# Performance work log

Measured on AMD Instinct MI355X. Metric: run time of the kernel, lower is better.

Reference implementation:

```python
import jax, jax.numpy as jnp
import numpy as np

N = 200000   # number of nodes / adj columns
F = 256      # input_features
L0 = 256     # layers[0]
L1 = 128     # layers[1]


def setup_inputs() -> dict:
    key = jax.random.key(0)
    k_adj, k_feat, k0, kb0, k1, kb1, ks = jax.random.split(key, 7)
    adj = jax.random.randint(k_adj, (1, N), 0, 2, dtype=jnp.int32)
    feature = jax.random.normal(k_feat, (N, F), dtype=jnp.float32)
    # MLP params: Linear(2F, L0) -> relu -> Linear(L0, L1) -> relu; score Linear(L1, 1, bias=False)
    W0 = jax.random.normal(k0, (2 * F, L0), dtype=jnp.float32) * 0.02
    b0 = jax.random.normal(kb0, (L0,), dtype=jnp.float32) * 0.02
    W1 = jax.random.normal(k1, (L0, L1), dtype=jnp.float32) * 0.02
    b1 = jax.random.normal(kb1, (L1,), dtype=jnp.float32) * 0.02
    w_score = jax.random.normal(ks, (L1, 1), dtype=jnp.float32) * 0.02
    return {"adj": adj, "feature": feature, "W0": W0, "b0": b0,
            "W1": W1, "b1": b1, "w_score": w_score}


def reference(adj, feature, W0, b0, W1, b1, w_score):
    # Original forward only processes row i=0 of adj (loop breaks immediately).
    # idx = nonzero columns of adj[0], plus sentinel -233 at the end.
    # Neighbor feature is feature[v] if v > 0 else zeros (so column 0 and the
    # sentinel both get a zero vector). Softmax is over the neighbor set (dim 0);
    # we realize this as a masked softmax over all N columns + 1 sentinel slot.
    n, f = feature.shape
    row = adj[0]
    mask = jnp.concatenate([row != 0, jnp.ones((1,), dtype=bool)])  # [n+1]
    # neighbor features: feature[v] for v=0..n-1 (v=0 -> zeros), plus zero sentinel row
    neigh = jnp.concatenate([feature.at[0].set(0.0),
                             jnp.zeros((1, f), feature.dtype)], axis=0)  # [n+1, f]
    self_feat = jnp.broadcast_to(feature[0], (n + 1, f))                 # [n+1, f]
    s = jnp.concatenate([self_feat, neigh], axis=1)                      # [n+1, 2f]
    h = jax.nn.relu(s @ W0 + b0)                                         # [n+1, L0]
    h = jax.nn.relu(h @ W1 + b1)                                         # [n+1, L1]
    scores = h @ w_score                                                 # [n+1, 1]
    scores = jnp.where(mask[:, None], scores, jnp.float32(-1e30))
    lk = jax.nn.softmax(scores, axis=0)
    return jnp.where(mask[:, None], lk, 0.0)
```

## Files before the change

### kernel.cpp

```cpp
#include <hip/hip_runtime.h>
#include <stdint.h>

#define NN   200000
#define NTOT 200001

typedef short bf16x8 __attribute__((ext_vector_type(8)));
typedef float f32x16 __attribute__((ext_vector_type(16)));

union FragU { bf16x8 v; unsigned q[4]; };

__device__ __forceinline__ unsigned bfrne(float x) {
  unsigned u = __float_as_uint(x);
  return (u + 0x7fffu + ((u >> 16) & 1u)) >> 16;
}
__device__ __forceinline__ unsigned pk2(float a, float b) {
  return bfrne(a) | (bfrne(b) << 16);
}
__device__ __forceinline__ unsigned shx32(unsigned x) {
  return (unsigned)__shfl_xor((int)x, 32, 64);
}

__global__ void gnn_prep(const float* __restrict__ feat, const float* __restrict__ W0,
                         const float* __restrict__ b0, const float* __restrict__ W1,
                         const float* __restrict__ b1, const float* __restrict__ wsc,
                         float* __restrict__ c0g, char* __restrict__ w0t,
                         char* __restrict__ w1t, float* __restrict__ scores,
                         float* __restrict__ S, int* __restrict__ cnt)
{
  const int tid = threadIdx.x;
  if (blockIdx.x == 0) {
    __shared__ float h0z[256];
    __shared__ float h1z[128];
    float a = b0[tid];
    for (int f = 0; f < 256; ++f) a = fmaf(feat[f], W0[f * 256 + tid], a);
    c0g[tid] = a;
    h0z[tid] = fmaxf(a, 0.f);
    __syncthreads();
    if (tid < 128) {
      float t = b1[tid];
      for (int k = 0; k < 256; ++k) t = fmaf(h0z[k], W1[k * 128 + tid], t);
      h1z[tid] = fmaxf(t, 0.f) * wsc[tid];
    }
    __syncthreads();
    if (tid == 0) {
      float sz = 0.f;
      for (int p = 0; p < 128; ++p) sz += h1z[p];
      scores[0]  = sz;
      scores[NN] = sz;
      *S = 0.f;
      *cnt = 0;
    }
  } else {
    int gid = (blockIdx.x - 1) * 256 + tid;
    if (gid < 8192) {
      int m = gid >> 5, a = gid & 31, k0 = a * 8;
      unsigned q0 = pk2(W0[(256 + k0 + 0) * 256 + m], W0[(256 + k0 + 1) * 256 + m]);
      unsigned q1 = pk2(W0[(256 + k0 + 2) * 256 + m], W0[(256 + k0 + 3) * 256 + m]);
      unsigned q2 = pk2(W0[(256 + k0 + 4) * 256 + m], W0[(256 + k0 + 5) * 256 + m]);
      unsigned q3 = pk2(W0[(256 + k0 + 6) * 256 + m], W0[(256 + k0 + 7) * 256 + m]);
      *(uint4*)(w0t + m * 512 + ((a ^ (m & 7)) << 4)) = make_uint4(q0, q1, q2, q3);
    } else if (gid < 12288) {
      int g2 = gid - 8192;
      int p = g2 >> 5, a = g2 & 31, k0 = a * 8;
      unsigned q0 = pk2(W1[(k0 + 0) * 128 + p], W1[(k0 + 1) * 128 + p]);
      unsigned q1 = pk2(W1[(k0 + 2) * 128 + p], W1[(k0 + 3) * 128 + p]);
      unsigned q2 = pk2(W1[(k0 + 4) * 128 + p], W1[(k0 + 5) * 128 + p]);
      unsigned q3 = pk2(W1[(k0 + 6) * 128 + p], W1[(k0 + 7) * 128 + p]);
      *(uint4*)(w1t + p * 512 + ((a ^ (p & 7)) << 4)) = make_uint4(q0, q1, q2, q3);
    }
  }
}

__global__ void gnn_compact(const int* __restrict__ adj, int* __restrict__ idx,
                            int* __restrict__ cnt)
{
  int i = blockIdx.x * blockDim.x + threadIdx.x;
  bool f = (i > 0) && (i < NN) && (adj[i] != 0);
  unsigned long long m = __ballot(f);
  int lane = threadIdx.x & 63;
  int tot = __popcll(m);
  int base = 0;
  if (lane == 0 && tot) base = atomicAdd(cnt, tot);
  base = __shfl(base, 0, 64);
  if (f) idx[base + __popcll(m & ((1ull << lane) - 1ull))] = i;
}

__global__ __launch_bounds__(256, 2) void
gnn_main(const float* __restrict__ feat, const char* __restrict__ w0t,
         const char* __restrict__ w1t, const float* __restrict__ c0g,
         const float* __restrict__ b1, const float* __restrict__ wsc,
         const int* __restrict__ idx, const int* __restrict__ cnt,
         float* __restrict__ scores)
{
  __shared__ __align__(16) char sW[2][32768];
  __shared__ float c0s[256];
  __shared__ float b1s[128];
  __shared__ float wss[128];

  const int M = *cnt;
  if ((int)blockIdx.x * 128 >= M) return;

  const int tid  = threadIdx.x;
  const int wave = tid >> 6, lane = tid & 63;
  const int h = lane >> 5, nl = lane & 31;

  const int slot = blockIdx.x * 128 + wave * 32 + nl;
  const int node = idx[min(slot, M - 1)];

  auto stage = [&](int buf, const char* gsrc) {
    const char* gp = gsrc + (wave << 13) + (lane << 4);
    char* lp = &sW[buf][wave << 13];
#pragma unroll
    for (int i = 0; i < 8; ++i)
      __builtin_amdgcn_global_load_lds(
          (const __attribute__((address_space(1))) unsigned*)(gp + (i << 10)),
          (__attribute__((address_space(3))) unsigned*)(lp + (i << 10)),
          16, 0, 0);
  };

  stage(0, w0t);

  FragU fB[16];
  const float4* frow = (const float4*)(feat + (size_t)node * 256);
#pragma unroll
  for (int kk = 0; kk < 16; ++kk) {
    float4 x = frow[4 * kk + 2 * h];
    float4 y = frow[4 * kk + 2 * h + 1];
    fB[kk].q[0] = pk2(x.x, x.y);
    fB[kk].q[1] = pk2(x.z, x.w);
    fB[kk].q[2] = pk2(y.x, y.y);
    fB[kk].q[3] = pk2(y.z, y.w);
  }

  c0s[tid] = c0g[tid];
  if (tid < 128) { b1s[tid] = b1[tid]; wss[tid] = wsc[tid]; }
  __syncthreads();

  unsigned h0p[8][8];
#pragma unroll
  for (int c = 0; c < 4; ++c) {
    stage((c + 1) & 1, (c < 3) ? (w0t + (c + 1) * 32768) : w1t);
    const char* Bp = sW[c & 1];
    f32x16 acc0, acc1;
#pragma unroll
    for (int i = 0; i < 16; ++i) { acc0[i] = 0.f; acc1[i] = 0.f; }
#pragma unroll
    for (int kk = 0; kk < 16; ++kk) {
      bf16x8 a0 = *(const bf16x8*)(Bp + nl * 512        + (((2 * kk + h) ^ (nl & 7)) << 4));
      bf16x8 a1 = *(const bf16x8*)(Bp + (32 + nl) * 512 + (((2 * kk + h) ^ (nl & 7)) << 4));
      acc0 = __builtin_amdgcn_mfma_f32_32x32x16_bf16(a0, fB[kk].v, acc0, 0, 0, 0);
      acc1 = __builtin_amdgcn_mfma_f32_32x32x16_bf16(a1, fB[kk].v, acc1, 0, 0, 0);
    }
#pragma unroll
    for (int t = 0; t < 2; ++t) {
      const f32x16& ac = t ? acc1 : acc0;
      const int tile = c * 2 + t, nb = tile * 32;
#pragma unroll
      for (int g = 0; g < 4; ++g) {
        float4 cv = *(const float4*)&c0s[nb + 8 * g + 4 * h];
        float v0 = fmaxf(ac[4 * g + 0] + cv.x, 0.f);
        float v1 = fmaxf(ac[4 * g + 1] + cv.y, 0.f);
        float v2 = fmaxf(ac[4 * g + 2] + cv.z, 0.f);
        float v3 = fmaxf(ac[4 * g + 3] + cv.w, 0.f);
        h0p[tile][2 * g + 0] = pk2(v0, v1);
        h0p[tile][2 * g + 1] = pk2(v2, v3);
      }
    }
    __syncthreads();
  }

  const bool hh = (h != 0);
#pragma unroll
  for (int tt = 0; tt < 8; ++tt) {
    unsigned o[8], s[8];
#pragma unroll
    for (int r = 0; r < 8; ++r) { o[r] = h0p[tt][r]; s[r] = shx32(o[r]); }
    h0p[tt][0] = hh ? s[2] : o[0];
    h0p[tt][1] = hh ? s[3] : o[1];
    h0p[tt][2] = hh ? o[2] : s[0];
    h0p[tt][3] = hh ? o[3] : s[1];
    h0p[tt][4] = hh ? s[6] : o[4];
    h0p[tt][5] = hh ? s[7] : o[5];
    h0p[tt][6] = hh ? o[6] : s[4];
    h0p[tt][7] = hh ? o[7] : s[5];
  }

  f32x16 acc2[4];
#pragma unroll
  for (int t = 0; t < 4; ++t)
#pragma unroll
    for (int i = 0; i < 16; ++i) acc2[t][i] = 0.f;

#pragma unroll
  for (int c2 = 0; c2 < 2; ++c2) {
    if (c2 == 0) stage(1, w1t + 32768);
    const char* Bp = sW[c2];
#pragma unroll
    for (int kk = 0; kk < 16; ++kk) {
      bf16x8 a0 = *(const bf16x8*)(Bp + nl * 512        + (((2 * kk + h) ^ (nl & 7)) << 4));
      bf16x8 a1 = *(const bf16x8*)(Bp + (32 + nl) * 512 + (((2 * kk + h) ^ (nl & 7)) << 4));
      FragU bb;
      const int tt = kk >> 1, p = kk & 1;
      bb.q[0] = h0p[tt][4 * p + 0];
      bb.q[1] = h0p[tt][4 * p + 1];
      bb.q[2] = h0p[tt][4 * p + 2];
      bb.q[3] = h0p[tt][4 * p + 3];
      acc2[c2 * 2 + 0] = __builtin_amdgcn_mfma_f32_32x32x16_bf16(a0, bb.v, acc2[c2 * 2 + 0], 0, 0, 0);
      acc2[c2 * 2 + 1] = __builtin_amdgcn_mfma_f32_32x32x16_bf16(a1, bb.v, acc2[c2 * 2 + 1], 0, 0, 0);
    }
    if (c2 == 0) __syncthreads();
  }

  float sc = 0.f;
#pragma unroll
  for (int pt = 0; pt < 4; ++pt) {
#pragma unroll
    for (int g = 0; g < 4; ++g) {
      float4 bv = *(const float4*)&b1s[pt * 32 + 8 * g + 4 * h];
      float4 wv = *(const float4*)&wss[pt * 32 + 8 * g + 4 * h];
      sc += fmaxf(acc2[pt][4 * g + 0] + bv.x, 0.f) * wv.x;
      sc += fmaxf(acc2[pt][4 * g + 1] + bv.y, 0.f) * wv.y;
      sc += fmaxf(acc2[pt][4 * g + 2] + bv.z, 0.f) * wv.z;
      sc += fmaxf(acc2[pt][4 * g + 3] + bv.w, 0.f) * wv.w;
    }
  }
  sc += __shfl_xor(sc, 32, 64);
  if (h == 0 && slot < M) scores[node] = sc;
}

__global__ void gnn_reduce(const int* __restrict__ adj, const float* __restrict__ scores,
                           float* __restrict__ S)
{
  float loc = 0.f;
  for (int i = blockIdx.x * blockDim.x + threadIdx.x; i <= NN;
       i += gridDim.x * blockDim.x) {
    bool m = (i == NN) || (adj[i] != 0);
    if (m) loc += expf(scores[i]);
  }
#pragma unroll
  for (int off = 32; off; off >>= 1) loc += __shfl_xor(loc, off, 64);
  __shared__ float part[4];
  if ((threadIdx.x & 63) == 0) part[threadIdx.x >> 6] = loc;
  __syncthreads();
  if (threadIdx.x == 0) atomicAdd(S, part[0] + part[1] + part[2] + part[3]);
}

__global__ void gnn_final(const int* __restrict__ adj, const float* __restrict__ scores,
                          const float* __restrict__ S, float* __restrict__ out)
{
  int i = blockIdx.x * blockDim.x + threadIdx.x;
  if (i > NN) return;
  bool m = (i == NN) || (adj[i] != 0);
  float Sv = *S;
  out[i] = m ? expf(scores[i]) / Sv : 0.f;
}

extern "C" void kernel_launch(void* const* d_in, const int* in_sizes, int n_in,
                              void* d_out, int out_size, void* d_ws, size_t ws_size,
                              hipStream_t stream)
{
  (void)in_sizes; (void)n_in; (void)out_size; (void)ws_size;
  const int*   adj  = (const int*)d_in[0];
  const float* feat = (const float*)d_in[1];
  const float* W0   = (const float*)d_in[2];
  const float* b0   = (const float*)d_in[3];
  const float* W1   = (const float*)d_in[4];
  const float* b1   = (const float*)d_in[5];
  const float* wsc  = (const float*)d_in[6];
  float* out = (float*)d_out;

  char* ws = (char*)d_ws;
  float* scores = (float*)ws;
  char*  w0t    = ws + 800256;
  char*  w1t    = ws + 931328;
  float* c0g    = (float*)(ws + 996864);
  float* S      = (float*)(ws + 997888);
  int*   cnt    = (int*)(ws + 997904);
  int*   idxb   = (int*)(ws + 997952);

  gnn_prep   <<<49,   256, 0, stream>>>(feat, W0, b0, W1, b1, wsc, c0g, w0t, w1t, scores, S, cnt);
  gnn_compact<<<782,  256, 0, stream>>>(adj, idxb, cnt);
  gnn_main   <<<1563, 256, 0, stream>>>(feat, w0t, w1t, c0g, b1, wsc, idxb, cnt, scores);
  gnn_reduce <<<512,  256, 0, stream>>>(adj, scores, S);
  gnn_final  <<<782,  256, 0, stream>>>(adj, scores, S, out);
}
```

Measured before the change: 365.3 us.

## Fuse softmax denominator into main kernel, permute W1 layout, batch compaction

```diff
diff --git a/kernel.cpp b/kernel.cpp
--- a/kernel.cpp
+++ b/kernel.cpp
@@ -16,16 +16,14 @@
 __device__ __forceinline__ unsigned pk2(float a, float b) {
   return bfrne(a) | (bfrne(b) << 16);
 }
-__device__ __forceinline__ unsigned shx32(unsigned x) {
-  return (unsigned)__shfl_xor((int)x, 32, 64);
-}
-
-__global__ void gnn_prep(const float* __restrict__ feat, const float* __restrict__ W0,
-                         const float* __restrict__ b0, const float* __restrict__ W1,
-                         const float* __restrict__ b1, const float* __restrict__ wsc,
-                         float* __restrict__ c0g, char* __restrict__ w0t,
-                         char* __restrict__ w1t, float* __restrict__ scores,
-                         float* __restrict__ S, int* __restrict__ cnt)
+
+__global__ void gnn_prep(const int* __restrict__ adj, const float* __restrict__ feat,
+                         const float* __restrict__ W0, const float* __restrict__ b0,
+                         const float* __restrict__ W1, const float* __restrict__ b1,
+                         const float* __restrict__ wsc, float* __restrict__ c0g,
+                         char* __restrict__ w0t, char* __restrict__ w1t,
+                         float* __restrict__ scores, float* __restrict__ S,
+                         int* __restrict__ cnt)
 {
   const int tid = threadIdx.x;
   if (blockIdx.x == 0) {
@@ -47,7 +45,7 @@
       for (int p = 0; p < 128; ++p) sz += h1z[p];
       scores[0]  = sz;
       scores[NN] = sz;
-      *S = 0.f;
+      *S = expf(sz) * (adj[0] != 0 ? 2.f : 1.f);
       *cnt = 0;
     }
   } else {
@@ -61,28 +59,52 @@
       *(uint4*)(w0t + m * 512 + ((a ^ (m & 7)) << 4)) = make_uint4(q0, q1, q2, q3);
     } else if (gid < 12288) {
       int g2 = gid - 8192;
-      int p = g2 >> 5, a = g2 & 31, k0 = a * 8;
-      unsigned q0 = pk2(W1[(k0 + 0) * 128 + p], W1[(k0 + 1) * 128 + p]);
-      unsigned q1 = pk2(W1[(k0 + 2) * 128 + p], W1[(k0 + 3) * 128 + p]);
-      unsigned q2 = pk2(W1[(k0 + 4) * 128 + p], W1[(k0 + 5) * 128 + p]);
-      unsigned q3 = pk2(W1[(k0 + 6) * 128 + p], W1[(k0 + 7) * 128 + p]);
+      int p = g2 >> 5, a = g2 & 31;
+      int base = 32 * (a >> 2) + 16 * ((a >> 1) & 1) + 4 * (a & 1);
+      unsigned q0 = pk2(W1[(base + 0)  * 128 + p], W1[(base + 1)  * 128 + p]);
+      unsigned q1 = pk2(W1[(base + 2)  * 128 + p], W1[(base + 3)  * 128 + p]);
+      unsigned q2 = pk2(W1[(base + 8)  * 128 + p], W1[(base + 9)  * 128 + p]);
+      unsigned q3 = pk2(W1[(base + 10) * 128 + p], W1[(base + 11) * 128 + p]);
       *(uint4*)(w1t + p * 512 + ((a ^ (p & 7)) << 4)) = make_uint4(q0, q1, q2, q3);
     }
   }
 }
 
-__global__ void gnn_compact(const int* __restrict__ adj, int* __restrict__ idx,
-                            int* __restrict__ cnt)
-{
-  int i = blockIdx.x * blockDim.x + threadIdx.x;
-  bool f = (i > 0) && (i < NN) && (adj[i] != 0);
-  unsigned long long m = __ballot(f);
-  int lane = threadIdx.x & 63;
-  int tot = __popcll(m);
-  int base = 0;
-  if (lane == 0 && tot) base = atomicAdd(cnt, tot);
-  base = __shfl(base, 0, 64);
-  if (f) idx[base + __popcll(m & ((1ull << lane) - 1ull))] = i;
+__global__ __launch_bounds__(1024) void
+gnn_compact(const int* __restrict__ adj, int* __restrict__ idx, int* __restrict__ cnt)
+{
+  __shared__ int wc[64];
+  __shared__ int bbase;
+  const int tid  = threadIdx.x;
+  const int wave = tid >> 6, lane = tid & 63;
+  const int R = blockIdx.x * 4096;
+
+  unsigned long long mk[4];
+#pragma unroll
+  for (int p = 0; p < 4; ++p) {
+    int i = R + p * 1024 + tid;
+    bool f = (i > 0) && (i < NN) && (adj[i] != 0);
+    mk[p] = __ballot(f);
+  }
+  if (lane == 0) {
+#pragma unroll
+    for (int p = 0; p < 4; ++p) wc[p * 16 + wave] = __popcll(mk[p]);
+  }
+  __syncthreads();
+  if (tid == 0) {
+    int run = 0;
+    for (int e = 0; e < 64; ++e) { int v = wc[e]; wc[e] = run; run += v; }
+    bbase = atomicAdd(cnt, run);
+  }
+  __syncthreads();
+  const int b0 = bbase;
+#pragma unroll
+  for (int p = 0; p < 4; ++p) {
+    if ((mk[p] >> lane) & 1ull) {
+      int i = R + p * 1024 + tid;
+      idx[b0 + wc[p * 16 + wave] + __popcll(mk[p] & ((1ull << lane) - 1ull))] = i;
+    }
+  }
 }
 
 __global__ __launch_bounds__(256, 2) void
@@ -90,12 +112,13 @@
          const char* __restrict__ w1t, const float* __restrict__ c0g,
          const float* __restrict__ b1, const float* __restrict__ wsc,
          const int* __restrict__ idx, const int* __restrict__ cnt,
-         float* __restrict__ scores)
+         float* __restrict__ scores, float* __restrict__ S)
 {
   __shared__ __align__(16) char sW[2][32768];
   __shared__ float c0s[256];
   __shared__ float b1s[128];
   __shared__ float wss[128];
+  __shared__ float wsum[4];
 
   const int M = *cnt;
   if ((int)blockIdx.x * 128 >= M) return;
@@ -167,22 +190,6 @@
       }
     }
     __syncthreads();
-  }
-
-  const bool hh = (h != 0);
-#pragma unroll
-  for (int tt = 0; tt < 8; ++tt) {
-    unsigned o[8], s[8];
-#pragma unroll
-    for (int r = 0; r < 8; ++r) { o[r] = h0p[tt][r]; s[r] = shx32(o[r]); }
-    h0p[tt][0] = hh ? s[2] : o[0];
-    h0p[tt][1] = hh ? s[3] : o[1];
-    h0p[tt][2] = hh ? o[2] : s[0];
-    h0p[tt][3] = hh ? o[3] : s[1];
-    h0p[tt][4] = hh ? s[6] : o[4];
-    h0p[tt][5] = hh ? s[7] : o[5];
-    h0p[tt][6] = hh ? o[6] : s[4];
-    h0p[tt][7] = hh ? o[7] : s[5];
   }
 
   f32x16 acc2[4];
@@ -226,23 +233,13 @@
   }
   sc += __shfl_xor(sc, 32, 64);
   if (h == 0 && slot < M) scores[node] = sc;
-}
-
-__global__ void gnn_reduce(const int* __restrict__ adj, const float* __restrict__ scores,
-                           float* __restrict__ S)
-{
-  float loc = 0.f;
-  for (int i = blockIdx.x * blockDim.x + threadIdx.x; i <= NN;
-       i += gridDim.x * blockDim.x) {
-    bool m = (i == NN) || (adj[i] != 0);
-    if (m) loc += expf(scores[i]);
-  }
-#pragma unroll
-  for (int off = 32; off; off >>= 1) loc += __shfl_xor(loc, off, 64);
-  __shared__ float part[4];
-  if ((threadIdx.x & 63) == 0) part[threadIdx.x >> 6] = loc;
-  __syncthreads();
-  if (threadIdx.x == 0) atomicAdd(S, part[0] + part[1] + part[2] + part[3]);
+
+  float ex = (slot < M) ? expf(sc) : 0.f;
+#pragma unroll
+  for (int off = 32; off; off >>= 1) ex += __shfl_xor(ex, off, 64);
+  if (lane == 0) wsum[wave] = ex * 0.5f;
+  __syncthreads();
+  if (tid == 0) atomicAdd(S, wsum[0] + wsum[1] + wsum[2] + wsum[3]);
 }
 
 __global__ void gnn_final(const int* __restrict__ adj, const float* __restrict__ scores,
@@ -278,9 +275,8 @@
   int*   cnt    = (int*)(ws + 997904);
   int*   idxb   = (int*)(ws + 997952);
 
-  gnn_prep   <<<49,   256, 0, stream>>>(feat, W0, b0, W1, b1, wsc, c0g, w0t, w1t, scores, S, cnt);
-  gnn_compact<<<782,  256, 0, stream>>>(adj, idxb, cnt);
-  gnn_main   <<<1563, 256, 0, stream>>>(feat, w0t, w1t, c0g, b1, wsc, idxb, cnt, scores);
-  gnn_reduce <<<512,  256, 0, stream>>>(adj, scores, S);
-  gnn_final  <<<782,  256, 0, stream>>>(adj, scores, S, out);
-}
+  gnn_prep   <<<49,   256,  0, stream>>>(adj, feat, W0, b0, W1, b1, wsc, c0g, w0t, w1t, scores, S, cnt);
+  gnn_compact<<<49,   1024, 0, stream>>>(adj, idxb, cnt);
+  gnn_main   <<<1563, 256,  0, stream>>>(feat, w0t, w1t, c0g, b1, wsc, idxb, cnt, scores, S);
+  gnn_final  <<<782,  256,  0, stream>>>(adj, scores, S, out);
+}
```

New measurement: 321.7 us. -11.9%, faster.
